# Optimization experiments

Hardware: AMD Instinct MI355X
Metric: run time of the kernel (lower is better)

Reference implementation:

```python
import jax, jax.numpy as jnp
import numpy as np

B, S, H = 64, 512, 768
A1, C1 = 100, 300          # token-attention and sentence-classifier hidden sizes
BETA = 1.0                 # soft_attention_beta
SLW, TLW, RLW = 1.0, 1.0, 0.01  # loss weights


def setup_inputs() -> dict:
    key = jax.random.key(0)
    ks = jax.random.split(key, 12)
    hidden_states = jax.random.normal(ks[0], (B, S, H), jnp.float32)
    # token_attention: Linear(H,100) -> Tanh -> Linear(100,1) -> Sigmoid
    w1 = jax.random.normal(ks[1], (H, A1), jnp.float32) * 0.02
    b1 = jnp.zeros((A1,), jnp.float32)
    w2 = jax.random.normal(ks[2], (A1, 1), jnp.float32) * 0.02
    b2 = jnp.zeros((1,), jnp.float32)
    # sentence_classification: Linear(H,300) -> Tanh -> Linear(300,1) -> Sigmoid
    sw1 = jax.random.normal(ks[3], (H, C1), jnp.float32) * 0.02
    sb1 = jnp.zeros((C1,), jnp.float32)
    sw2 = jax.random.normal(ks[4], (C1, 1), jnp.float32) * 0.02
    sb2 = jnp.zeros((1,), jnp.float32)
    offset_mapping = jax.random.randint(ks[5], (B, S, 2), 0, 4).astype(jnp.int32)
    offset_mapping = offset_mapping.at[:, 0, 0].set(0)  # first token starts a word
    # labels in {-1, 0, 1}; -1 = ignore
    labels = jax.random.randint(ks[6], (B, S), -1, 2).astype(jnp.float32)
    return {
        "hidden_states": hidden_states,
        "w1": w1, "b1": b1, "w2": w2, "b2": b2,
        "sw1": sw1, "sb1": sb1, "sw2": sw2, "sb2": sb2,
        "labels": labels,
        "offset_mapping": offset_mapping,
    }


def _forward(hidden_states, w1, b1, w2, b2, sw1, sb1, sw2, sb2, labels, offset_mapping):
    # token attention scores in (0,1): [B, S]
    token_att = jax.nn.sigmoid(
        jnp.tanh(hidden_states @ w1 + b1) @ w2 + b2
    )[..., 0]

    # ragged per-word subword max-pooling (segment-max along the sequence)
    not_subword = offset_mapping[:, :, 0] == 0                 # [B, S] word starts
    seg = jnp.maximum(jnp.cumsum(not_subword.astype(jnp.int32), axis=1) - 1, 0)

    def _seg_max(vals, seg_ids):
        return jax.ops.segment_max(vals, seg_ids, num_segments=S)

    segmax = jax.vmap(_seg_max)(token_att, seg)                # [B, S] per-word max
    word_att = jnp.where(not_subword, jnp.take_along_axis(segmax, seg, axis=1), 0.0)

    # mask: labeled tokens that are word starts
    token_mask = ((labels != -1) & not_subword).astype(token_att.dtype)
    masked = word_att * token_mask                              # token_logits [B, S]

    # beta-normalized soft attention pooling over hidden states
    p = masked ** BETA
    att_norm = p / jnp.sum(p, axis=1, keepdims=True)            # [B, S]
    pooled = jnp.einsum("bsh,bs->bh", hidden_states, att_norm)  # [B, H]

    sent = jax.nn.sigmoid(jnp.tanh(pooled @ sw1 + sb1) @ sw2 + sb2)  # [B, 1]

    # losses (MSE with reduction='sum')
    sentence_labels = jnp.max(labels, axis=1, keepdims=True)    # [B, 1]
    sentence_loss = jnp.sum((sent - sentence_labels) ** 2)
    zero_labels = jnp.where(labels != -1, labels, 0.0)
    token_loss = jnp.sum((masked - zero_labels) ** 2)
    ones_masked = jnp.where(masked == 0, 1.0, masked)
    reg_a = jnp.sum(jnp.min(ones_masked, axis=1, keepdims=True) ** 2)
    reg_b = jnp.sum((jnp.max(masked, axis=1, keepdims=True) - sentence_labels) ** 2)
    total = SLW * sentence_loss + TLW * token_loss + RLW * (reg_a + reg_b)
    return total, sentence_loss, token_loss, reg_a, reg_b, masked, sent


def reference(hidden_states, w1, b1, w2, b2, sw1, sb1, sw2, sb2, labels, offset_mapping):
    return _forward(hidden_states, w1, b1, w2, b2, sw1, sb1, sw2, sb2,
                    labels, offset_mapping)
```

## Files before the change

kernel.cpp:

```cpp
#include <hip/hip_runtime.h>
#include <math.h>

#define BB 64
#define SS 512
#define HH 768
#define AA1 100
#define CC1 300

typedef __bf16 bf16x8 __attribute__((ext_vector_type(8)));
typedef float f32x4 __attribute__((ext_vector_type(4)));

#ifndef __has_builtin
#define __has_builtin(x) 0
#endif
#if __has_builtin(__builtin_amdgcn_global_load_lds)
#define HAVE_GLL 1
#else
#define HAVE_GLL 0
#endif

#define AS1 __attribute__((address_space(1)))
#define AS3 __attribute__((address_space(3)))

__global__ __launch_bounds__(256) void k_prep(const float* __restrict__ w1,
                                              __bf16* __restrict__ w1i) {
    int idx = blockIdx.x * 256 + threadIdx.x;
    int j = idx % 112;
    int r = idx / 112;
    int e = r & 7, g = r >> 3;
    int k = (g >> 2) * 32 + (g & 3) * 8 + e;
    float v = (j < AA1) ? w1[k * AA1 + j] : 0.f;
    w1i[((size_t)g * 112 + j) * 8 + e] = (__bf16)v;
}

__global__ __launch_bounds__(256) void k_token_att(
        const float* __restrict__ hs, const __bf16* __restrict__ w1i,
        const float* __restrict__ b1, const float* __restrict__ w2,
        const float* __restrict__ b2, float* __restrict__ token_att) {
    __shared__ __attribute__((aligned(16))) float lA[2048];
    __shared__ __attribute__((aligned(16))) __bf16 lB[3584];

    const int tid = threadIdx.x;
    const int tok0 = blockIdx.x * 64;
    const int w = tid >> 6, lane = tid & 63;
    const int q = lane >> 4, ln = lane & 15;
    const int t = w * 16 + ln;

    f32x4 acc[7];
#pragma unroll
    for (int n = 0; n < 7; n++) acc[n] = (f32x4){0.f, 0.f, 0.f, 0.f};

    const int p0 = (2 * q) ^ (ln & 7);
    const int p1 = (2 * q + 1) ^ (ln & 7);

    for (int kt = 0; kt < 24; kt++) {
        const int ko = kt * 32;
        {
            int i0 = tid;
            int t0 = i0 >> 3, c0 = (i0 & 7) ^ (t0 & 7);
            const float* g0 = hs + (size_t)(tok0 + t0) * HH + ko + c0 * 4;
            int i1 = tid + 256;
            int t1 = i1 >> 3, c1 = (i1 & 7) ^ (t1 & 7);
            const float* g1 = hs + (size_t)(tok0 + t1) * HH + ko + c1 * 4;
            const __bf16* gb0 = w1i + (size_t)kt * 3584 + (size_t)tid * 8;
#if HAVE_GLL
            __builtin_amdgcn_global_load_lds((AS1 void*)g0,
                    (AS3 void*)(lA + (w * 64) * 4), 16, 0, 0);
            __builtin_amdgcn_global_load_lds((AS1 void*)g1,
                    (AS3 void*)(lA + (256 + w * 64) * 4), 16, 0, 0);
            __builtin_amdgcn_global_load_lds((AS1 void*)gb0,
                    (AS3 void*)(lB + (w * 64) * 8), 16, 0, 0);
            if (w < 3) {
                const __bf16* gb1 = w1i + (size_t)kt * 3584 + (size_t)(tid + 256) * 8;
                __builtin_amdgcn_global_load_lds((AS1 void*)gb1,
                        (AS3 void*)(lB + (256 + w * 64) * 8), 16, 0, 0);
            }
#else
            *(f32x4*)&lA[i0 * 4] = *(const f32x4*)g0;
            *(f32x4*)&lA[i1 * 4] = *(const f32x4*)g1;
            *(bf16x8*)&lB[(size_t)tid * 8] = *(const bf16x8*)gb0;
            if (tid < 192) {
                const __bf16* gb1 = w1i + (size_t)kt * 3584 + (size_t)(tid + 256) * 8;
                *(bf16x8*)&lB[(size_t)(tid + 256) * 8] = *(const bf16x8*)gb1;
            }
#endif
        }
        __syncthreads();
        f32x4 a0 = *(f32x4*)&lA[(t * 8 + p0) * 4];
        f32x4 a1 = *(f32x4*)&lA[(t * 8 + p1) * 4];
        bf16x8 af;
        af[0] = (__bf16)a0[0]; af[1] = (__bf16)a0[1];
        af[2] = (__bf16)a0[2]; af[3] = (__bf16)a0[3];
        af[4] = (__bf16)a1[0]; af[5] = (__bf16)a1[1];
        af[6] = (__bf16)a1[2]; af[7] = (__bf16)a1[3];
#pragma unroll
        for (int n = 0; n < 7; n++) {
            bf16x8 bf = *(bf16x8*)&lB[((size_t)q * 112 + n * 16 + ln) * 8];
            acc[n] = __builtin_amdgcn_mfma_f32_16x16x32_bf16(af, bf, acc[n], 0, 0, 0);
        }
        __syncthreads();
    }

    float s0 = 0.f, s1 = 0.f, s2 = 0.f, s3 = 0.f;
#pragma unroll
    for (int n = 0; n < 7; n++) {
        int j = n * 16 + ln;
        if (j < AA1) {
            float bj = b1[j], wj = w2[j];
            s0 += tanhf(acc[n][0] + bj) * wj;
            s1 += tanhf(acc[n][1] + bj) * wj;
            s2 += tanhf(acc[n][2] + bj) * wj;
            s3 += tanhf(acc[n][3] + bj) * wj;
        }
    }
#pragma unroll
    for (int off = 1; off < 16; off <<= 1) {
        s0 += __shfl_xor(s0, off);
        s1 += __shfl_xor(s1, off);
        s2 += __shfl_xor(s2, off);
        s3 += __shfl_xor(s3, off);
    }
    if (ln == 0) {
        float bb = b2[0];
        int base = tok0 + w * 16 + q * 4;
        token_att[base + 0] = 1.f / (1.f + expf(-(s0 + bb)));
        token_att[base + 1] = 1.f / (1.f + expf(-(s1 + bb)));
        token_att[base + 2] = 1.f / (1.f + expf(-(s2 + bb)));
        token_att[base + 3] = 1.f / (1.f + expf(-(s3 + bb)));
    }
}

__global__ __launch_bounds__(512) void k_mask(
        const float* __restrict__ token_att, const float* __restrict__ labels,
        const int* __restrict__ offm, float* __restrict__ masked_out,
        float* __restrict__ cw_g, short* __restrict__ cs_g,
        int* __restrict__ nnz_g, float* __restrict__ inv_g,
        float4* __restrict__ stats_g) {
    __shared__ int smax[512];
    __shared__ int wscan[8];
    __shared__ int wscan2[8];
    __shared__ float wred[5][8];

    const int b = blockIdx.x, s = threadIdx.x;
    const int lane = s & 63, wv = s >> 6;
    const int ns = (offm[(b * SS + s) * 2] == 0) ? 1 : 0;

    int v = ns;
#pragma unroll
    for (int off = 1; off < 64; off <<= 1) {
        int o = __shfl_up(v, off);
        if (lane >= off) v += o;
    }
    if (lane == 63) wscan[wv] = v;
    smax[s] = 0;
    __syncthreads();
    int woff = 0;
    for (int i = 0; i < 8; i++) woff += (i < wv) ? wscan[i] : 0;
    const int seg = max(v + woff - 1, 0);

    const float ta = token_att[b * SS + s];
    atomicMax(&smax[seg], __float_as_int(ta));
    __syncthreads();

    const float wa = ns ? __int_as_float(smax[seg]) : 0.f;
    const float lab = labels[b * SS + s];
    const float m = (lab != -1.f && ns) ? wa : 0.f;
    masked_out[b * SS + s] = m;

    const float zl = (lab != -1.f) ? lab : 0.f;
    const float tl = (m - zl) * (m - zl);
    const float ones = (m == 0.f) ? 1.f : m;

    float r0 = m, r1 = tl, r2 = m, r3 = ones, r4 = lab;
#pragma unroll
    for (int off = 32; off > 0; off >>= 1) {
        r0 += __shfl_xor(r0, off);
        r1 += __shfl_xor(r1, off);
        r2 = fmaxf(r2, __shfl_xor(r2, off));
        r3 = fminf(r3, __shfl_xor(r3, off));
        r4 = fmaxf(r4, __shfl_xor(r4, off));
    }
    if (lane == 0) {
        wred[0][wv] = r0; wred[1][wv] = r1; wred[2][wv] = r2;
        wred[3][wv] = r3; wred[4][wv] = r4;
    }

    const int nz = (m != 0.f) ? 1 : 0;
    int v2 = nz;
#pragma unroll
    for (int off = 1; off < 64; off <<= 1) {
        int o = __shfl_up(v2, off);
        if (lane >= off) v2 += o;
    }
    if (lane == 63) wscan2[wv] = v2;
    __syncthreads();

    int woff2 = 0;
    for (int i = 0; i < 8; i++) woff2 += (i < wv) ? wscan2[i] : 0;
    if (nz) {
        int pos = v2 + woff2 - 1;
        cw_g[b * SS + pos] = m;
        cs_g[b * SS + pos] = (short)s;
    }
    if (s == 0) {
        float att = 0.f, tokl = 0.f, maxm = -1e30f, minone = 1e30f, slab = -1e30f;
        int nnz = 0;
        for (int i = 0; i < 8; i++) {
            att += wred[0][i]; tokl += wred[1][i];
            maxm = fmaxf(maxm, wred[2][i]);
            minone = fminf(minone, wred[3][i]);
            slab = fmaxf(slab, wred[4][i]);
            nnz += wscan2[i];
        }
        nnz_g[b] = nnz;
        inv_g[b] = 1.f / att;
        stats_g[b] = make_float4(tokl, maxm, minone, slab);
    }
}

__global__ __launch_bounds__(256) void k_pool(
        const float* __restrict__ hs, const float* __restrict__ cw_g,
        const short* __restrict__ cs_g, const int* __restrict__ nnz_g,
        const float* __restrict__ inv_g, float* __restrict__ pooled) {
    __shared__ float w[SS];
    __shared__ short idx[SS];
    const int b = blockIdx.x, g = blockIdx.y, tid = threadIdx.x;
    const int nnz = nnz_g[b];
    for (int i = tid; i < nnz; i += 256) {
        w[i] = cw_g[b * SS + i];
        idx[i] = cs_g[b * SS + i];
    }
    __syncthreads();
    const int h = g * 256 + tid;
    const float* hsb = hs + (size_t)b * SS * HH + h;
    float a0 = 0.f, a1 = 0.f, a2 = 0.f, a3 = 0.f;
    float a4 = 0.f, a5 = 0.f, a6 = 0.f, a7 = 0.f;
    int i = 0;
    for (; i + 8 <= nnz; i += 8) {
        a0 += hsb[(size_t)idx[i + 0] * HH] * w[i + 0];
        a1 += hsb[(size_t)idx[i + 1] * HH] * w[i + 1];
        a2 += hsb[(size_t)idx[i + 2] * HH] * w[i + 2];
        a3 += hsb[(size_t)idx[i + 3] * HH] * w[i + 3];
        a4 += hsb[(size_t)idx[i + 4] * HH] * w[i + 4];
        a5 += hsb[(size_t)idx[i + 5] * HH] * w[i + 5];
        a6 += hsb[(size_t)idx[i + 6] * HH] * w[i + 6];
        a7 += hsb[(size_t)idx[i + 7] * HH] * w[i + 7];
    }
    for (; i < nnz; i++) a0 += hsb[(size_t)idx[i] * HH] * w[i];
    float acc = ((a0 + a1) + (a2 + a3)) + ((a4 + a5) + (a6 + a7));
    pooled[b * HH + h] = acc * inv_g[b];
}

__global__ __launch_bounds__(320) void k_sentfinal(
        const float* __restrict__ pooled, const float4* __restrict__ stats_g,
        const float* __restrict__ sw1, const float* __restrict__ sb1,
        const float* __restrict__ sw2, const float* __restrict__ sb2,
        float* __restrict__ sent_out, float* __restrict__ out) {
    __shared__ float p[HH];
    __shared__ float wsum[5];
    const int b = blockIdx.x, tid = threadIdx.x;
    const int lane = tid & 63, wv = tid >> 6;
    for (int i = tid; i < HH; i += 320) p[i] = pooled[b * HH + i];
    __syncthreads();

    float tt = 0.f;
    if (tid < CC1) {
        float z = sb1[tid];
#pragma unroll 8
        for (int k = 0; k < HH; k++) z += p[k] * sw1[k * CC1 + tid];
        tt = tanhf(z) * sw2[tid];
    }
#pragma unroll
    for (int off = 32; off > 0; off >>= 1) tt += __shfl_xor(tt, off);
    if (lane == 0) wsum[wv] = tt;
    __syncthreads();
    if (tid == 0) {
        float zsum = wsum[0] + wsum[1] + wsum[2] + wsum[3] + wsum[4];
        float sv = 1.f / (1.f + expf(-(zsum + sb2[0])));
        sent_out[b] = sv;
        float4 st = stats_g[b];
        float vs = sv - st.w; vs *= vs;
        float ra = st.z * st.z;
        float rb = st.y - st.w; rb *= rb;
        atomicAdd(&out[1], vs);
        atomicAdd(&out[2], st.x);
        atomicAdd(&out[3], ra);
        atomicAdd(&out[4], rb);
        atomicAdd(&out[0], vs + st.x + 0.01f * (ra + rb));
    }
}

extern "C" void kernel_launch(void* const* d_in, const int* in_sizes, int n_in,
                              void* d_out, int out_size, void* d_ws, size_t ws_size,
                              hipStream_t stream) {
    const float* hs  = (const float*)d_in[0];
    const float* w1  = (const float*)d_in[1];
    const float* b1  = (const float*)d_in[2];
    const float* w2  = (const float*)d_in[3];
    const float* b2  = (const float*)d_in[4];
    const float* sw1 = (const float*)d_in[5];
    const float* sb1 = (const float*)d_in[6];
    const float* sw2 = (const float*)d_in[7];
    const float* sb2 = (const float*)d_in[8];
    const float* labels = (const float*)d_in[9];
    const int*   offm   = (const int*)d_in[10];

    float* out = (float*)d_out;
    float* ws  = (float*)d_ws;

    float*  token_att = ws;
    __bf16* w1i    = (__bf16*)(ws + 32768);
    float*  cw     = ws + 32768 + 43008;
    short*  cs     = (short*)(cw + 32768);
    int*    nnz    = (int*)(cw + 32768 + 16384);
    float*  inv    = (float*)(nnz + 64);
    float4* stats  = (float4*)(inv + 64);
    float*  pooled = inv + 64 + 256;

    float* masked_out = out + 5;
    float* sent_out   = out + 5 + BB * SS;

    hipMemsetAsync(out, 0, 5 * sizeof(float), stream);
    hipLaunchKernelGGL(k_prep, dim3(336), dim3(256), 0, stream, w1, w1i);
    hipLaunchKernelGGL(k_token_att, dim3(512), dim3(256), 0, stream,
                       hs, w1i, b1, w2, b2, token_att);
    hipLaunchKernelGGL(k_mask, dim3(BB), dim3(512), 0, stream,
                       token_att, labels, offm, masked_out,
                       cw, cs, nnz, inv, stats);
    hipLaunchKernelGGL(k_pool, dim3(BB, 3), dim3(256), 0, stream,
                       hs, cw, cs, nnz, inv, pooled);
    hipLaunchKernelGGL(k_sentfinal, dim3(BB), dim3(320), 0, stream,
                       pooled, stats, sw1, sb1, sw2, sb2, sent_out, out);
}
```

Measured before the change: 246.9 us.

## Double token tile per block, fuse pooling with sentence head, drop memset

The token-attention GEMM kernel now gives each block 128 tokens, so each wave runs two MFMA row tiles that share every B-fragment load, and the grid halves to 256 blocks. The pooling and sentence-classifier kernels are merged into one 512-thread kernel per batch that keeps the pooled vector in LDS, removing a launch and the global round trip for pooled. The output memset is replaced by zeroing inside k_mask. In exchange, pooling now uses only 64 blocks instead of 192, which cuts parallelism for the gather over hidden_states, and the GEMM has fewer blocks and higher register pressure.

```diff
diff --git a/kernel.cpp b/kernel.cpp
--- a/kernel.cpp
+++ b/kernel.cpp
@@ -37,37 +37,43 @@
         const float* __restrict__ hs, const __bf16* __restrict__ w1i,
         const float* __restrict__ b1, const float* __restrict__ w2,
         const float* __restrict__ b2, float* __restrict__ token_att) {
-    __shared__ __attribute__((aligned(16))) float lA[2048];
+    __shared__ __attribute__((aligned(16))) float lA[4096];
     __shared__ __attribute__((aligned(16))) __bf16 lB[3584];
 
     const int tid = threadIdx.x;
-    const int tok0 = blockIdx.x * 64;
+    const int tok0 = blockIdx.x * 128;
     const int w = tid >> 6, lane = tid & 63;
     const int q = lane >> 4, ln = lane & 15;
-    const int t = w * 16 + ln;
-
-    f32x4 acc[7];
-#pragma unroll
-    for (int n = 0; n < 7; n++) acc[n] = (f32x4){0.f, 0.f, 0.f, 0.f};
+    const int t0 = w * 32 + ln;
+    const int t1 = t0 + 16;
+
+    f32x4 acc0[7], acc1[7];
+#pragma unroll
+    for (int n = 0; n < 7; n++) {
+        acc0[n] = (f32x4){0.f, 0.f, 0.f, 0.f};
+        acc1[n] = (f32x4){0.f, 0.f, 0.f, 0.f};
+    }
 
     const int p0 = (2 * q) ^ (ln & 7);
     const int p1 = (2 * q + 1) ^ (ln & 7);
 
     for (int kt = 0; kt < 24; kt++) {
         const int ko = kt * 32;
+#pragma unroll
+        for (int it = 0; it < 4; it++) {
+            int i = tid + it * 256;
+            int tt = i >> 3, c = (i & 7) ^ (tt & 7);
+            const float* g = hs + (size_t)(tok0 + tt) * HH + ko + c * 4;
+#if HAVE_GLL
+            __builtin_amdgcn_global_load_lds((AS1 void*)g,
+                    (AS3 void*)(lA + (it * 256 + w * 64) * 4), 16, 0, 0);
+#else
+            *(f32x4*)&lA[i * 4] = *(const f32x4*)g;
+#endif
+        }
         {
-            int i0 = tid;
-            int t0 = i0 >> 3, c0 = (i0 & 7) ^ (t0 & 7);
-            const float* g0 = hs + (size_t)(tok0 + t0) * HH + ko + c0 * 4;
-            int i1 = tid + 256;
-            int t1 = i1 >> 3, c1 = (i1 & 7) ^ (t1 & 7);
-            const float* g1 = hs + (size_t)(tok0 + t1) * HH + ko + c1 * 4;
             const __bf16* gb0 = w1i + (size_t)kt * 3584 + (size_t)tid * 8;
 #if HAVE_GLL
-            __builtin_amdgcn_global_load_lds((AS1 void*)g0,
-                    (AS3 void*)(lA + (w * 64) * 4), 16, 0, 0);
-            __builtin_amdgcn_global_load_lds((AS1 void*)g1,
-                    (AS3 void*)(lA + (256 + w * 64) * 4), 16, 0, 0);
             __builtin_amdgcn_global_load_lds((AS1 void*)gb0,
                     (AS3 void*)(lB + (w * 64) * 8), 16, 0, 0);
             if (w < 3) {
@@ -76,8 +82,6 @@
                         (AS3 void*)(lB + (256 + w * 64) * 8), 16, 0, 0);
             }
 #else
-            *(f32x4*)&lA[i0 * 4] = *(const f32x4*)g0;
-            *(f32x4*)&lA[i1 * 4] = *(const f32x4*)g1;
             *(bf16x8*)&lB[(size_t)tid * 8] = *(const bf16x8*)gb0;
             if (tid < 192) {
                 const __bf16* gb1 = w1i + (size_t)kt * 3584 + (size_t)(tid + 256) * 8;
@@ -86,47 +90,61 @@
 #endif
         }
         __syncthreads();
-        f32x4 a0 = *(f32x4*)&lA[(t * 8 + p0) * 4];
-        f32x4 a1 = *(f32x4*)&lA[(t * 8 + p1) * 4];
-        bf16x8 af;
-        af[0] = (__bf16)a0[0]; af[1] = (__bf16)a0[1];
-        af[2] = (__bf16)a0[2]; af[3] = (__bf16)a0[3];
-        af[4] = (__bf16)a1[0]; af[5] = (__bf16)a1[1];
-        af[6] = (__bf16)a1[2]; af[7] = (__bf16)a1[3];
+        f32x4 a00 = *(f32x4*)&lA[(t0 * 8 + p0) * 4];
+        f32x4 a01 = *(f32x4*)&lA[(t0 * 8 + p1) * 4];
+        f32x4 a10 = *(f32x4*)&lA[(t1 * 8 + p0) * 4];
+        f32x4 a11 = *(f32x4*)&lA[(t1 * 8 + p1) * 4];
+        bf16x8 af0, af1;
+#pragma unroll
+        for (int e = 0; e < 4; e++) {
+            af0[e] = (__bf16)a00[e]; af0[e + 4] = (__bf16)a01[e];
+            af1[e] = (__bf16)a10[e]; af1[e + 4] = (__bf16)a11[e];
+        }
 #pragma unroll
         for (int n = 0; n < 7; n++) {
             bf16x8 bf = *(bf16x8*)&lB[((size_t)q * 112 + n * 16 + ln) * 8];
-            acc[n] = __builtin_amdgcn_mfma_f32_16x16x32_bf16(af, bf, acc[n], 0, 0, 0);
+            acc0[n] = __builtin_amdgcn_mfma_f32_16x16x32_bf16(af0, bf, acc0[n], 0, 0, 0);
+            acc1[n] = __builtin_amdgcn_mfma_f32_16x16x32_bf16(af1, bf, acc1[n], 0, 0, 0);
         }
         __syncthreads();
     }
 
     float s0 = 0.f, s1 = 0.f, s2 = 0.f, s3 = 0.f;
+    float u0 = 0.f, u1 = 0.f, u2 = 0.f, u3 = 0.f;
 #pragma unroll
     for (int n = 0; n < 7; n++) {
         int j = n * 16 + ln;
         if (j < AA1) {
             float bj = b1[j], wj = w2[j];
-            s0 += tanhf(acc[n][0] + bj) * wj;
-            s1 += tanhf(acc[n][1] + bj) * wj;
-            s2 += tanhf(acc[n][2] + bj) * wj;
-            s3 += tanhf(acc[n][3] + bj) * wj;
+            s0 += tanhf(acc0[n][0] + bj) * wj;
+            s1 += tanhf(acc0[n][1] + bj) * wj;
+            s2 += tanhf(acc0[n][2] + bj) * wj;
+            s3 += tanhf(acc0[n][3] + bj) * wj;
+            u0 += tanhf(acc1[n][0] + bj) * wj;
+            u1 += tanhf(acc1[n][1] + bj) * wj;
+            u2 += tanhf(acc1[n][2] + bj) * wj;
+            u3 += tanhf(acc1[n][3] + bj) * wj;
         }
     }
 #pragma unroll
     for (int off = 1; off < 16; off <<= 1) {
-        s0 += __shfl_xor(s0, off);
-        s1 += __shfl_xor(s1, off);
-        s2 += __shfl_xor(s2, off);
-        s3 += __shfl_xor(s3, off);
+        s0 += __shfl_xor(s0, off); s1 += __shfl_xor(s1, off);
+        s2 += __shfl_xor(s2, off); s3 += __shfl_xor(s3, off);
+        u0 += __shfl_xor(u0, off); u1 += __shfl_xor(u1, off);
+        u2 += __shfl_xor(u2, off); u3 += __shfl_xor(u3, off);
     }
     if (ln == 0) {
         float bb = b2[0];
-        int base = tok0 + w * 16 + q * 4;
-        token_att[base + 0] = 1.f / (1.f + expf(-(s0 + bb)));
-        token_att[base + 1] = 1.f / (1.f + expf(-(s1 + bb)));
-        token_att[base + 2] = 1.f / (1.f + expf(-(s2 + bb)));
-        token_att[base + 3] = 1.f / (1.f + expf(-(s3 + bb)));
+        int base0 = tok0 + w * 32 + q * 4;
+        int base1 = base0 + 16;
+        token_att[base0 + 0] = 1.f / (1.f + expf(-(s0 + bb)));
+        token_att[base0 + 1] = 1.f / (1.f + expf(-(s1 + bb)));
+        token_att[base0 + 2] = 1.f / (1.f + expf(-(s2 + bb)));
+        token_att[base0 + 3] = 1.f / (1.f + expf(-(s3 + bb)));
+        token_att[base1 + 0] = 1.f / (1.f + expf(-(u0 + bb)));
+        token_att[base1 + 1] = 1.f / (1.f + expf(-(u1 + bb)));
+        token_att[base1 + 2] = 1.f / (1.f + expf(-(u2 + bb)));
+        token_att[base1 + 3] = 1.f / (1.f + expf(-(u3 + bb)));
     }
 }
 
@@ -135,7 +153,7 @@
         const int* __restrict__ offm, float* __restrict__ masked_out,
         float* __restrict__ cw_g, short* __restrict__ cs_g,
         int* __restrict__ nnz_g, float* __restrict__ inv_g,
-        float4* __restrict__ stats_g) {
+        float4* __restrict__ stats_g, float* __restrict__ out) {
     __shared__ int smax[512];
     __shared__ int wscan[8];
     __shared__ int wscan2[8];
@@ -143,6 +161,7 @@
 
     const int b = blockIdx.x, s = threadIdx.x;
     const int lane = s & 63, wv = s >> 6;
+    if (b == 0 && s < 5) out[s] = 0.f;
     const int ns = (offm[(b * SS + s) * 2] == 0) ? 1 : 0;
 
     int v = ns;
@@ -218,56 +237,55 @@
     }
 }
 
-__global__ __launch_bounds__(256) void k_pool(
+__global__ __launch_bounds__(512) void k_poolsent(
         const float* __restrict__ hs, const float* __restrict__ cw_g,
         const short* __restrict__ cs_g, const int* __restrict__ nnz_g,
-        const float* __restrict__ inv_g, float* __restrict__ pooled) {
-    __shared__ float w[SS];
-    __shared__ short idx[SS];
-    const int b = blockIdx.x, g = blockIdx.y, tid = threadIdx.x;
-    const int nnz = nnz_g[b];
-    for (int i = tid; i < nnz; i += 256) {
-        w[i] = cw_g[b * SS + i];
-        idx[i] = cs_g[b * SS + i];
-    }
-    __syncthreads();
-    const int h = g * 256 + tid;
-    const float* hsb = hs + (size_t)b * SS * HH + h;
-    float a0 = 0.f, a1 = 0.f, a2 = 0.f, a3 = 0.f;
-    float a4 = 0.f, a5 = 0.f, a6 = 0.f, a7 = 0.f;
-    int i = 0;
-    for (; i + 8 <= nnz; i += 8) {
-        a0 += hsb[(size_t)idx[i + 0] * HH] * w[i + 0];
-        a1 += hsb[(size_t)idx[i + 1] * HH] * w[i + 1];
-        a2 += hsb[(size_t)idx[i + 2] * HH] * w[i + 2];
-        a3 += hsb[(size_t)idx[i + 3] * HH] * w[i + 3];
-        a4 += hsb[(size_t)idx[i + 4] * HH] * w[i + 4];
-        a5 += hsb[(size_t)idx[i + 5] * HH] * w[i + 5];
-        a6 += hsb[(size_t)idx[i + 6] * HH] * w[i + 6];
-        a7 += hsb[(size_t)idx[i + 7] * HH] * w[i + 7];
-    }
-    for (; i < nnz; i++) a0 += hsb[(size_t)idx[i] * HH] * w[i];
-    float acc = ((a0 + a1) + (a2 + a3)) + ((a4 + a5) + (a6 + a7));
-    pooled[b * HH + h] = acc * inv_g[b];
-}
-
-__global__ __launch_bounds__(320) void k_sentfinal(
-        const float* __restrict__ pooled, const float4* __restrict__ stats_g,
+        const float* __restrict__ inv_g, const float4* __restrict__ stats_g,
         const float* __restrict__ sw1, const float* __restrict__ sb1,
         const float* __restrict__ sw2, const float* __restrict__ sb2,
         float* __restrict__ sent_out, float* __restrict__ out) {
-    __shared__ float p[HH];
-    __shared__ float wsum[5];
+    __shared__ float w[SS];
+    __shared__ short idx[SS];
+    __shared__ float pool[HH];
+    __shared__ float wsum[8];
+
     const int b = blockIdx.x, tid = threadIdx.x;
     const int lane = tid & 63, wv = tid >> 6;
-    for (int i = tid; i < HH; i += 320) p[i] = pooled[b * HH + i];
+    const int nnz = nnz_g[b];
+    if (tid < nnz) { w[tid] = cw_g[b * SS + tid]; idx[tid] = cs_g[b * SS + tid]; }
+    __syncthreads();
+
+    const float* hsb = hs + (size_t)b * SS * HH;
+    const bool hi = (tid < 256);
+    float a[8], c[8];
+#pragma unroll
+    for (int u = 0; u < 8; u++) { a[u] = 0.f; c[u] = 0.f; }
+    int i = 0;
+    for (; i + 8 <= nnz; i += 8) {
+#pragma unroll
+        for (int u = 0; u < 8; u++)
+            a[u] += hsb[(size_t)idx[i + u] * HH + tid] * w[i + u];
+        if (hi) {
+#pragma unroll
+            for (int u = 0; u < 8; u++)
+                c[u] += hsb[(size_t)idx[i + u] * HH + 512 + tid] * w[i + u];
+        }
+    }
+    for (; i < nnz; i++) {
+        a[0] += hsb[(size_t)idx[i] * HH + tid] * w[i];
+        if (hi) c[0] += hsb[(size_t)idx[i] * HH + 512 + tid] * w[i];
+    }
+    const float inv = inv_g[b];
+    pool[tid] = (((a[0] + a[1]) + (a[2] + a[3])) + ((a[4] + a[5]) + (a[6] + a[7]))) * inv;
+    if (hi)
+        pool[512 + tid] = (((c[0] + c[1]) + (c[2] + c[3])) + ((c[4] + c[5]) + (c[6] + c[7]))) * inv;
     __syncthreads();
 
     float tt = 0.f;
     if (tid < CC1) {
         float z = sb1[tid];
 #pragma unroll 8
-        for (int k = 0; k < HH; k++) z += p[k] * sw1[k * CC1 + tid];
+        for (int k = 0; k < HH; k++) z += pool[k] * sw1[k * CC1 + tid];
         tt = tanhf(z) * sw2[tid];
     }
 #pragma unroll
@@ -315,20 +333,17 @@
     int*    nnz    = (int*)(cw + 32768 + 16384);
     float*  inv    = (float*)(nnz + 64);
     float4* stats  = (float4*)(inv + 64);
-    float*  pooled = inv + 64 + 256;
 
     float* masked_out = out + 5;
     float* sent_out   = out + 5 + BB * SS;
 
-    hipMemsetAsync(out, 0, 5 * sizeof(float), stream);
     hipLaunchKernelGGL(k_prep, dim3(336), dim3(256), 0, stream, w1, w1i);
-    hipLaunchKernelGGL(k_token_att, dim3(512), dim3(256), 0, stream,
+    hipLaunchKernelGGL(k_token_att, dim3(256), dim3(256), 0, stream,
                        hs, w1i, b1, w2, b2, token_att);
     hipLaunchKernelGGL(k_mask, dim3(BB), dim3(512), 0, stream,
                        token_att, labels, offm, masked_out,
-                       cw, cs, nnz, inv, stats);
-    hipLaunchKernelGGL(k_pool, dim3(BB, 3), dim3(256), 0, stream,
-                       hs, cw, cs, nnz, inv, pooled);
-    hipLaunchKernelGGL(k_sentfinal, dim3(BB), dim3(320), 0, stream,
-                       pooled, stats, sw1, sb1, sw2, sb2, sent_out, out);
-}
+                       cw, cs, nnz, inv, stats, out);
+    hipLaunchKernelGGL(k_poolsent, dim3(BB), dim3(512), 0, stream,
+                       hs, cw, cs, nnz, inv, stats,
+                       sw1, sb1, sw2, sb2, sent_out, out);
+}
```

Result: no change. 246.6 us (-0.1%).
